# Performance work log

Measured on AMD Instinct MI355X. Metric: run time of the kernel, lower is better.

The kernel has to match this reference:

```python
import jax, jax.numpy as jnp
from jax import lax
import numpy as np

FEAT = 256
B = 16
T = 4096
BETA = 1.0


def setup_inputs() -> dict:
    key = jax.random.key(0)
    k0, k1, k2 = jax.random.split(key, 3)
    encoder_outputs = jax.random.normal(k0, (B, T, FEAT), dtype=jnp.float32)
    # Conv1d weight: (out_ch, in_ch, kernel)
    conv_w = jax.random.normal(k1, (FEAT, FEAT, 5), dtype=jnp.float32) * 0.02
    conv_b = jnp.zeros((FEAT,), dtype=jnp.float32)
    lin_w = jax.random.normal(k2, (FEAT, 1), dtype=jnp.float32) * 0.05
    lin_b = jnp.zeros((1,), dtype=jnp.float32)
    return {"encoder_outputs": encoder_outputs, "conv_w": conv_w,
            "conv_b": conv_b, "lin_w": lin_w, "lin_b": lin_b}


def _alphas(x, conv_w, conv_b, lin_w, lin_b):
    # x: [B, T, D] -> alphas [B, T]
    xc = jnp.transpose(x, (0, 2, 1))  # NCH
    y = lax.conv_general_dilated(xc, conv_w, window_strides=(1,),
                                 padding='SAME',
                                 dimension_numbers=('NCH', 'OIH', 'NCH'))
    y = y + conv_b[None, :, None]
    y = jnp.transpose(y, (0, 2, 1))  # [B, T, D]
    return jax.nn.sigmoid(y @ lin_w + lin_b)[..., 0]  # [B, T]


def _cif_single(alpha, h, beta):
    # alpha: [T], h: [T, D]  integrate-and-fire scan
    D = h.shape[-1]
    Tlen = alpha.shape[0]

    def step(carry, inp):
        acc, hacc = carry
        a, hu = inp
        acc_new = acc + a
        fire = acc_new >= beta
        a1 = 1.0 - acc          # mass to complete current segment
        c = hacc + a1 * hu      # emitted segment vector (if fired)
        a2 = a - a1             # leftover mass starting next segment
        acc_out = jnp.where(fire, a2, acc_new)
        hacc_out = jnp.where(fire, a2 * hu, hacc + a * hu)
        return (acc_out, hacc_out), (fire, jnp.where(fire, c, jnp.zeros_like(c)))

    init = (jnp.zeros((), h.dtype), jnp.zeros((D,), h.dtype))
    (acc_f, hacc_f), (fires, cs) = lax.scan(step, init, (alpha, h))

    # pack fired emissions densely; non-fired steps scatter into dump slot Tlen
    idx = jnp.cumsum(fires.astype(jnp.int32)) - 1
    idx = jnp.where(fires, idx, Tlen)
    out = jnp.zeros((Tlen + 1, D), h.dtype).at[idx].add(cs)[:Tlen]
    n = fires.sum().astype(jnp.int32)
    # if no segment fired, emit the final accumulator (torch: c=[h_accum[-1]])
    out = out.at[0].set(jnp.where(n == 0, hacc_f, out[0]))
    n = jnp.maximum(n, 1)
    return out, n


def reference(encoder_outputs, conv_w, conv_b, lin_w, lin_b):
    alphas = _alphas(encoder_outputs, conv_w, conv_b, lin_w, lin_b)  # [B, T]
    out_c, len_tensor = jax.vmap(lambda a, h: _cif_single(a, h, BETA))(
        alphas, encoder_outputs)
    return out_c, len_tensor
```

## Files before the change

kernel.cpp:

```cpp
#include <hip/hip_runtime.h>
#include <math.h>

#define FEAT 256
#define NB   16
#define TLEN 4096
#define NROWS (NB * TLEN)

#define OFF_WEFF 0
#define OFF_BEFF 1280
#define OFF_P    2048
#define OFF_W1   (OFF_P + 5 * NROWS)
#define OFF_W2   (OFF_W1 + NROWS)
#define OFF_FPOS (OFF_W2 + NROWS)
#define OFF_NF   (OFF_FPOS + NROWS)
#define OFF_PART (OFF_NF + 16)

__global__ __launch_bounds__(256) void weff1_kernel(
    const float* __restrict__ conv_w, const float* __restrict__ lin_w,
    float* __restrict__ ws) {
  int ob = blockIdx.x % 5, oc = blockIdx.x / 5;
  int idx = ob * 256 + threadIdx.x;
  float acc = 0.f;
  int o0 = oc * 32;
#pragma unroll 8
  for (int o = o0; o < o0 + 32; ++o)
    acc = fmaf(conv_w[o * (FEAT * 5) + idx], lin_w[o], acc);
  ws[OFF_PART + oc * 1280 + idx] = acc;
}

__global__ __launch_bounds__(256) void weff2_kernel(
    const float* __restrict__ conv_b, const float* __restrict__ lin_w,
    const float* __restrict__ lin_b, float* __restrict__ ws) {
  if (blockIdx.x < 5) {
    int idx = blockIdx.x * 256 + threadIdx.x;
    float acc = 0.f;
#pragma unroll
    for (int c = 0; c < 8; ++c) acc += ws[OFF_PART + c * 1280 + idx];
    int i = idx / 5, k = idx - i * 5;
    ws[OFF_WEFF + k * FEAT + i] = acc;
  } else {
    __shared__ float red[256];
    red[threadIdx.x] = conv_b[threadIdx.x] * lin_w[threadIdx.x];
    __syncthreads();
    for (int s = 128; s > 0; s >>= 1) {
      if (threadIdx.x < s) red[threadIdx.x] += red[threadIdx.x + s];
      __syncthreads();
    }
    if (threadIdx.x == 0) ws[OFF_BEFF] = red[0] + lin_b[0];
  }
}

__global__ __launch_bounds__(256) void pdot_kernel(
    const float* __restrict__ x, float* __restrict__ ws) {
  int tid  = threadIdx.x;
  int wave = tid >> 6, l = tid & 63;
  int row  = blockIdx.x * 32 + wave * 8 + (l >> 3);
  int l8   = l & 7;
  const float* xr = x + (size_t)row * FEAT + l8 * 4;
  float p[5] = {0.f, 0.f, 0.f, 0.f, 0.f};
#pragma unroll
  for (int pass = 0; pass < 8; ++pass) {
    float4 xv = *(const float4*)(xr + pass * 32);
#pragma unroll
    for (int k = 0; k < 5; ++k) {
      float4 w4 = *(const float4*)(ws + OFF_WEFF + k * FEAT + pass * 32 + l8 * 4);
      p[k] = fmaf(xv.x, w4.x, fmaf(xv.y, w4.y,
              fmaf(xv.z, w4.z, fmaf(xv.w, w4.w, p[k]))));
    }
  }
#pragma unroll
  for (int k = 0; k < 5; ++k) {
    p[k] += __shfl_xor(p[k], 1);
    p[k] += __shfl_xor(p[k], 2);
    p[k] += __shfl_xor(p[k], 4);
  }
  if (l8 == 0) {
#pragma unroll
    for (int k = 0; k < 5; ++k) ws[OFF_P + (size_t)k * NROWS + row] = p[k];
  }
}

#define PAD(t) ((t) + ((t) >> 4))
__global__ __launch_bounds__(256) void scan_kernel(
    float* __restrict__ ws, float* __restrict__ out) {
  const int b = blockIdx.x;
  __shared__ float  s_alpha[TLEN + (TLEN >> 4)];
  __shared__ double s_part[256];
  const float b_eff = ws[OFF_BEFF];
  const float* Pb = ws + OFF_P + (size_t)b * TLEN;

  for (int j = 0; j < TLEN / 256; ++j) {
    int t = j * 256 + threadIdx.x;
    float z = b_eff;
#pragma unroll
    for (int k = 0; k < 5; ++k) {
      int tt = t + k - 2;
      if (tt >= 0 && tt < TLEN) z += Pb[(size_t)k * NROWS + tt];
    }
    s_alpha[PAD(t)] = 1.f / (1.f + expf(-z));
  }
  __syncthreads();

  const int base = threadIdx.x * 16;
  double run = 0.0;
#pragma unroll
  for (int r = 0; r < 16; ++r) run += (double)s_alpha[PAD(base + r)];
  s_part[threadIdx.x] = run;
  __syncthreads();
  for (int s = 1; s < 256; s <<= 1) {
    double add = (threadIdx.x >= s) ? s_part[threadIdx.x - s] : 0.0;
    __syncthreads();
    if (threadIdx.x >= s) s_part[threadIdx.x] += add;
    __syncthreads();
  }
  double offset = threadIdx.x ? s_part[threadIdx.x - 1] : 0.0;

  double Sprev = offset;
  double Fprev = floor(Sprev);
  float* w1 = ws + OFF_W1 + b * TLEN;
  float* w2 = ws + OFF_W2 + b * TLEN;
  int* fpos = (int*)ws + OFF_FPOS + b * TLEN;
  double runl = 0.0;
#pragma unroll
  for (int r = 0; r < 16; ++r) {
    int t = base + r;
    runl += (double)s_alpha[PAD(t)];
    double St = offset + runl;
    double Ft = floor(St);
    w1[t] = (float)(fmin(St, Fprev + 1.0) - Sprev);
    if (Ft > Fprev) {
      w2[t] = (float)(St - Ft);
      fpos[(int)Ft - 1] = t;
    }
    Sprev = St; Fprev = Ft;
  }
  if (threadIdx.x == 255) {
    int n = (int)Fprev;
    ((int*)ws)[OFF_NF + b] = n;
    out[(size_t)NROWS * FEAT + b] = (float)(n > 0 ? n : 1);
  }
}

__global__ __launch_bounds__(256) void emit_kernel(
    const float* __restrict__ x, const float* __restrict__ ws,
    float* __restrict__ out) {
  int gtid = blockIdx.x * 256 + threadIdx.x;
  int row  = gtid >> 6;
  int lane = gtid & 63;
  int b = row >> 12;
  int j = row & (TLEN - 1);
  int n = ((const int*)ws)[OFF_NF + b];
  int keep = n > 0 ? n : 1;
  float4 acc = make_float4(0.f, 0.f, 0.f, 0.f);
  if (j < keep) {
    const int* fpos = (const int*)ws + OFF_FPOS + b * TLEN;
    int t_lo = j ? fpos[j - 1] : 0;
    int t_hi = (j < n) ? fpos[j] : TLEN - 1;
    const float* w1 = ws + OFF_W1 + b * TLEN;
    const float* w2 = ws + OFF_W2 + b * TLEN;
    for (int t = t_lo; t <= t_hi; ++t) {
      float w = (j && t == t_lo) ? w2[t] : w1[t];
      float4 xv = *(const float4*)(x + ((size_t)b * TLEN + t) * FEAT + lane * 4);
      acc.x = fmaf(w, xv.x, acc.x);
      acc.y = fmaf(w, xv.y, acc.y);
      acc.z = fmaf(w, xv.z, acc.z);
      acc.w = fmaf(w, xv.w, acc.w);
    }
  }
  *(float4*)(out + (size_t)row * FEAT + lane * 4) = acc;
}

extern "C" void kernel_launch(void* const* d_in, const int* in_sizes, int n_in,
                              void* d_out, int out_size, void* d_ws, size_t ws_size,
                              hipStream_t stream) {
  const float* x      = (const float*)d_in[0];
  const float* conv_w = (const float*)d_in[1];
  const float* conv_b = (const float*)d_in[2];
  const float* lin_w  = (const float*)d_in[3];
  const float* lin_b  = (const float*)d_in[4];
  float* out = (float*)d_out;
  float* ws  = (float*)d_ws;

  hipLaunchKernelGGL(weff1_kernel, dim3(40), dim3(256), 0, stream,
                     conv_w, lin_w, ws);
  hipLaunchKernelGGL(weff2_kernel, dim3(6), dim3(256), 0, stream,
                     conv_b, lin_w, lin_b, ws);
  hipLaunchKernelGGL(pdot_kernel, dim3(NROWS / 32), dim3(256), 0, stream, x, ws);
  hipLaunchKernelGGL(scan_kernel, dim3(NB), dim3(256), 0, stream, ws, out);
  hipLaunchKernelGGL(emit_kernel, dim3(NROWS / 4), dim3(256), 0, stream, x, ws, out);
}
```

Baseline: 165.4 us.

## Split per-batch scan into two-pass chunked scan across 256 blocks

The single 16-block scan kernel, which computed sigmoid alphas and a double-precision prefix sum per batch, is replaced by two kernels launched with 256 blocks each. The first computes alphas and per-chunk sums; the second adds chunk offsets, does an in-block scan and writes fire weights and positions. This spreads the serial scan over far more CUs to cut the latency of a poorly occupied stage, at the cost of an extra launch and a round trip of alphas through global memory.

```diff
diff --git a/kernel.cpp b/kernel.cpp
--- a/kernel.cpp
+++ b/kernel.cpp
@@ -14,6 +14,8 @@
 #define OFF_FPOS (OFF_W2 + NROWS)
 #define OFF_NF   (OFF_FPOS + NROWS)
 #define OFF_PART (OFF_NF + 16)
+#define OFF_ALPHA (OFF_PART + 8 * 1280)
+#define OFF_CSUM (OFF_ALPHA + NROWS)
 
 __global__ __launch_bounds__(256) void weff1_kernel(
     const float* __restrict__ conv_w, const float* __restrict__ lin_w,
@@ -80,62 +82,62 @@
   }
 }
 
-#define PAD(t) ((t) + ((t) >> 4))
-__global__ __launch_bounds__(256) void scan_kernel(
-    float* __restrict__ ws, float* __restrict__ out) {
-  const int b = blockIdx.x;
-  __shared__ float  s_alpha[TLEN + (TLEN >> 4)];
-  __shared__ double s_part[256];
-  const float b_eff = ws[OFF_BEFF];
-  const float* Pb = ws + OFF_P + (size_t)b * TLEN;
+__global__ __launch_bounds__(256) void scanA_kernel(float* __restrict__ ws) {
+  const int b = blockIdx.x >> 4, chunk = blockIdx.x & 15;
+  const int tid = threadIdx.x;
+  const int t = chunk * 256 + tid;
+  float z = ws[OFF_BEFF];
+#pragma unroll
+  for (int k = 0; k < 5; ++k) {
+    int tt = t + k - 2;
+    if (tt >= 0 && tt < TLEN) z += ws[OFF_P + (size_t)k * NROWS + b * TLEN + tt];
+  }
+  float a = 1.f / (1.f + expf(-z));
+  ws[OFF_ALPHA + b * TLEN + t] = a;
 
-  for (int j = 0; j < TLEN / 256; ++j) {
-    int t = j * 256 + threadIdx.x;
-    float z = b_eff;
-#pragma unroll
-    for (int k = 0; k < 5; ++k) {
-      int tt = t + k - 2;
-      if (tt >= 0 && tt < TLEN) z += Pb[(size_t)k * NROWS + tt];
-    }
-    s_alpha[PAD(t)] = 1.f / (1.f + expf(-z));
-  }
-  __syncthreads();
-
-  const int base = threadIdx.x * 16;
-  double run = 0.0;
-#pragma unroll
-  for (int r = 0; r < 16; ++r) run += (double)s_alpha[PAD(base + r)];
-  s_part[threadIdx.x] = run;
+  __shared__ double sS[256];
+  sS[tid] = (double)a;
   __syncthreads();
   for (int s = 1; s < 256; s <<= 1) {
-    double add = (threadIdx.x >= s) ? s_part[threadIdx.x - s] : 0.0;
+    double add = (tid >= s) ? sS[tid - s] : 0.0;
     __syncthreads();
-    if (threadIdx.x >= s) s_part[threadIdx.x] += add;
+    sS[tid] += add;
     __syncthreads();
   }
-  double offset = threadIdx.x ? s_part[threadIdx.x - 1] : 0.0;
+  if (tid == 255)
+    ((double*)ws)[OFF_CSUM / 2 + b * 16 + chunk] = sS[255];
+}
 
-  double Sprev = offset;
-  double Fprev = floor(Sprev);
-  float* w1 = ws + OFF_W1 + b * TLEN;
-  float* w2 = ws + OFF_W2 + b * TLEN;
-  int* fpos = (int*)ws + OFF_FPOS + b * TLEN;
-  double runl = 0.0;
-#pragma unroll
-  for (int r = 0; r < 16; ++r) {
-    int t = base + r;
-    runl += (double)s_alpha[PAD(t)];
-    double St = offset + runl;
-    double Ft = floor(St);
-    w1[t] = (float)(fmin(St, Fprev + 1.0) - Sprev);
-    if (Ft > Fprev) {
-      w2[t] = (float)(St - Ft);
-      fpos[(int)Ft - 1] = t;
-    }
-    Sprev = St; Fprev = Ft;
+__global__ __launch_bounds__(256) void scanB_kernel(
+    float* __restrict__ ws, float* __restrict__ out) {
+  const int b = blockIdx.x >> 4, chunk = blockIdx.x & 15;
+  const int tid = threadIdx.x;
+  const int t = chunk * 256 + tid;
+  const double* csum = (const double*)ws + OFF_CSUM / 2 + b * 16;
+  double offset = 0.0;
+  for (int c = 0; c < chunk; ++c) offset += csum[c];
+
+  double a = (double)ws[OFF_ALPHA + b * TLEN + t];
+  __shared__ double sS[256];
+  sS[tid] = a;
+  __syncthreads();
+  for (int s = 1; s < 256; s <<= 1) {
+    double add = (tid >= s) ? sS[tid - s] : 0.0;
+    __syncthreads();
+    sS[tid] += add;
+    __syncthreads();
   }
-  if (threadIdx.x == 255) {
-    int n = (int)Fprev;
+  double St = offset + sS[tid];
+  double Sp = tid ? offset + sS[tid - 1] : offset;
+  double Ft = floor(St), Fp = floor(Sp);
+
+  ws[OFF_W1 + b * TLEN + t] = (float)(fmin(St, Fp + 1.0) - Sp);
+  if (Ft > Fp) {
+    ws[OFF_W2 + b * TLEN + t] = (float)(St - Ft);
+    ((int*)ws)[OFF_FPOS + b * TLEN + (int)Ft - 1] = t;
+  }
+  if (chunk == 15 && tid == 255) {
+    int n = (int)Ft;
     ((int*)ws)[OFF_NF + b] = n;
     out[(size_t)NROWS * FEAT + b] = (float)(n > 0 ? n : 1);
   }
@@ -186,6 +188,7 @@
   hipLaunchKernelGGL(weff2_kernel, dim3(6), dim3(256), 0, stream,
                      conv_b, lin_w, lin_b, ws);
   hipLaunchKernelGGL(pdot_kernel, dim3(NROWS / 32), dim3(256), 0, stream, x, ws);
-  hipLaunchKernelGGL(scan_kernel, dim3(NB), dim3(256), 0, stream, ws, out);
+  hipLaunchKernelGGL(scanA_kernel, dim3(NB * 16), dim3(256), 0, stream, ws);
+  hipLaunchKernelGGL(scanB_kernel, dim3(NB * 16), dim3(256), 0, stream, ws, out);
   hipLaunchKernelGGL(emit_kernel, dim3(NROWS / 4), dim3(256), 0, stream, x, ws, out);
 }
```

Measured after the change: 154.8 us, median of 2. 6.4% less time.
